# Kernel optimization log

Hardware: AMD Instinct MI355X
Metric: run time of the kernel (lower is better)

Reference implementation:

```python
import jax, jax.numpy as jnp
import numpy as np

B, M = 1024, 200000
D_IN, DIM, D_OUT = 256, 128, 10
T = 1.0
EPS = 1e-7


def setup_inputs() -> dict:
    key = jax.random.key(0)
    k1, k2, k3, k4, k5 = jax.random.split(key, 5)
    x = jax.random.normal(k1, (B, D_IN), dtype=jnp.float32)
    y = jax.random.randint(k2, (B,), 0, D_OUT)
    candidate_x = jax.random.normal(k3, (M, D_IN), dtype=jnp.float32)
    candidate_y = jax.random.randint(k4, (M,), 0, D_OUT)
    W_enc = jax.random.normal(k5, (DIM, D_IN), dtype=jnp.float32) * (1.0 / np.sqrt(D_IN))
    b_enc = jnp.zeros((DIM,), dtype=jnp.float32)
    return {"x": x, "y": y, "candidate_x": candidate_x, "candidate_y": candidate_y,
            "W_enc": W_enc, "b_enc": b_enc, "is_train": 0}


def reference(x, y, candidate_x, candidate_y, W_enc, b_enc, is_train):
    # eval path (is_train == 0): no candidate subsampling, no diagonal masking
    h = x @ W_enc.T + b_enc            # [B, DIM]
    hc = candidate_x @ W_enc.T + b_enc  # [M, DIM]
    # pairwise L2 distance (cdist, p=2)
    sq = jnp.sum(h * h, axis=-1, keepdims=True) + jnp.sum(hc * hc, axis=-1)[None, :] \
         - 2.0 * (h @ hc.T)            # [B, M]
    dist = jnp.sqrt(jnp.maximum(sq, 0.0)) / T
    p = jax.nn.softmax(-dist, axis=-1)  # [B, M]
    y1h = jax.nn.one_hot(candidate_y, D_OUT, dtype=h.dtype)  # [M, D_OUT]
    logits = p @ y1h                    # [B, D_OUT]
    return jnp.log(logits + EPS)
```

## Files before the change

kernel.cpp:

```cpp
#include <hip/hip_runtime.h>
#include <hip/hip_bf16.h>
#include <math.h>

#define B_N   1024
#define M_N   200000
#define DIN   256
#define DIMN  128
#define DOUT  10
#define EPS_F 1e-7f
#define M_PAD 200064
#define NBY   1563
#define NBX_C 1563
#define NBX_X 8
#define CTILES 8
#define NGY   196

typedef __bf16 bf16_t;
typedef __bf16 bf16x8 __attribute__((ext_vector_type(8)));
typedef float  f32x4  __attribute__((ext_vector_type(4)));


__global__ void prep_kernel(const float* __restrict__ W, bf16_t* __restrict__ Wb,
                            const int* __restrict__ cy, int* __restrict__ hist){
    __shared__ int h[DOUT];
    if (threadIdx.x < DOUT) h[threadIdx.x] = 0;
    __syncthreads();
    int gid = blockIdx.x*256 + threadIdx.x;
    if (gid < DIMN*DIN) Wb[gid] = (bf16_t)W[gid];
    for (int i = gid; i < M_N; i += 256*256)
        atomicAdd(&h[cy[i]], 1);
    __syncthreads();
    if (threadIdx.x < DOUT) atomicAdd(&hist[threadIdx.x*16], h[threadIdx.x]);
}

__global__ void prefix_kernel(const int* __restrict__ hist, int* __restrict__ cs){
    if (threadIdx.x == 0 && blockIdx.x == 0){
        int acc = 0;
        for (int c = 0; c < DOUT; ++c){ cs[c] = acc; acc += hist[c*16]; }
        cs[DOUT] = acc;
    }
}


__global__ __launch_bounds__(256) void encode_kernel(
    const float* __restrict__ cx, const float* __restrict__ xx,
    const bf16_t* __restrict__ Wb,
    bf16_t* __restrict__ hcb, bf16_t* __restrict__ hb,
    float* __restrict__ hcn, float* __restrict__ hn,
    const int* __restrict__ cy, int* __restrict__ counters,
    const int* __restrict__ cs)
{
    __shared__ bf16_t As[128][136];
    __shared__ int   posL[128];
    __shared__ float nbuf[128][2];
    __shared__ int   cntL[DOUT], baseL[DOUT];
    const int tid = threadIdx.x;

    const bool isC = (blockIdx.x < NBX_C);
    const float* __restrict__ src = isC ? cx : xx;
    bf16_t* __restrict__ out   = isC ? hcb : hb;
    float*  __restrict__ onorm = isC ? hcn : hn;
    const int N  = isC ? M_N : B_N;
    const int r0 = (isC ? blockIdx.x : blockIdx.x - NBX_C)*128;

    int myc = -1, myrank = 0;
    if (isC){
        if (tid < DOUT) cntL[tid] = 0;
        __syncthreads();
        if (tid < 128 && r0 + tid < N){
            myc = cy[r0 + tid];
            myrank = atomicAdd(&cntL[myc], 1);
        }
        __syncthreads();
        if (tid < DOUT && cntL[tid] > 0)
            baseL[tid] = atomicAdd(&counters[tid*16], cntL[tid]);
        __syncthreads();
    }
    if (tid < 128)
        posL[tid] = (myc >= 0) ? (cs[myc] + baseL[myc] + myrank) : (r0 + tid);

    const int lane = tid & 63, wid = tid >> 6;
    const int wr = wid >> 1, wc = wid & 1;
    const int l15 = lane & 15, quad = lane >> 4;
    const int cbase = wc*64;

    float4 Rlo[8], Rhi[8];
    #pragma unroll
    for (int i = 0; i < 8; ++i){
        int idx = i*256 + tid, row = idx >> 4, col = (idx & 15)*8;
        int rr = r0 + row; if (rr > N-1) rr = N-1;
        const float4* p4 = (const float4*)(src + (size_t)rr*DIN + col);
        Rlo[i] = p4[0]; Rhi[i] = p4[1];
    }
    #pragma unroll
    for (int i = 0; i < 8; ++i){
        int idx = i*256 + tid, row = idx >> 4, col = (idx & 15)*8;
        float4 f0 = Rlo[i], f1 = Rhi[i];
        bf16x8 v;
        v[0]=(bf16_t)f0.x; v[1]=(bf16_t)f0.y; v[2]=(bf16_t)f0.z; v[3]=(bf16_t)f0.w;
        v[4]=(bf16_t)f1.x; v[5]=(bf16_t)f1.y; v[6]=(bf16_t)f1.z; v[7]=(bf16_t)f1.w;
        *(bf16x8*)&As[row][col] = v;
    }
    __syncthreads();
    #pragma unroll
    for (int i = 0; i < 8; ++i){
        int idx = i*256 + tid, row = idx >> 4, col = (idx & 15)*8;
        int rr = r0 + row; if (rr > N-1) rr = N-1;
        const float4* p4 = (const float4*)(src + (size_t)rr*DIN + 128 + col);
        Rlo[i] = p4[0]; Rhi[i] = p4[1];
    }

    f32x4 acc[4][4] = {};
    #pragma unroll
    for (int ks = 0; ks < 4; ++ks){
        const int k = ks*32 + quad*8;
        bf16x8 a[4], b[4];
        #pragma unroll
        for (int rt = 0; rt < 4; ++rt)
            a[rt] = *(const bf16x8*)&As[wr*64 + rt*16 + l15][k];
        #pragma unroll
        for (int ct = 0; ct < 4; ++ct)
            b[ct] = *(const bf16x8*)(Wb + (size_t)(cbase + ct*16 + l15)*DIN + k);
        #pragma unroll
        for (int rt = 0; rt < 4; ++rt)
            #pragma unroll
            for (int ct = 0; ct < 4; ++ct)
                acc[rt][ct] = __builtin_amdgcn_mfma_f32_16x16x32_bf16(a[rt], b[ct], acc[rt][ct], 0, 0, 0);
    }
    __syncthreads();
    #pragma unroll
    for (int i = 0; i < 8; ++i){
        int idx = i*256 + tid, row = idx >> 4, col = (idx & 15)*8;
        float4 f0 = Rlo[i], f1 = Rhi[i];
        bf16x8 v;
        v[0]=(bf16_t)f0.x; v[1]=(bf16_t)f0.y; v[2]=(bf16_t)f0.z; v[3]=(bf16_t)f0.w;
        v[4]=(bf16_t)f1.x; v[5]=(bf16_t)f1.y; v[6]=(bf16_t)f1.z; v[7]=(bf16_t)f1.w;
        *(bf16x8*)&As[row][col] = v;
    }
    __syncthreads();
    #pragma unroll
    for (int ks = 0; ks < 4; ++ks){
        const int k = ks*32 + quad*8;
        bf16x8 a[4], b[4];
        #pragma unroll
        for (int rt = 0; rt < 4; ++rt)
            a[rt] = *(const bf16x8*)&As[wr*64 + rt*16 + l15][k];
        #pragma unroll
        for (int ct = 0; ct < 4; ++ct)
            b[ct] = *(const bf16x8*)(Wb + (size_t)(cbase + ct*16 + l15)*DIN + 128 + k);
        #pragma unroll
        for (int rt = 0; rt < 4; ++rt)
            #pragma unroll
            for (int ct = 0; ct < 4; ++ct)
                acc[rt][ct] = __builtin_amdgcn_mfma_f32_16x16x32_bf16(a[rt], b[ct], acc[rt][ct], 0, 0, 0);
    }

    float np[4][4];
    #pragma unroll
    for (int rt = 0; rt < 4; ++rt)
        #pragma unroll
        for (int r = 0; r < 4; ++r){
            float s = 0.f;
            #pragma unroll
            for (int ct = 0; ct < 4; ++ct){ float v = acc[rt][ct][r]; s += v*v; }
            np[rt][r] = s;
        }
    #pragma unroll
    for (int m = 1; m < 16; m <<= 1)
        #pragma unroll
        for (int rt = 0; rt < 4; ++rt)
            #pragma unroll
            for (int r = 0; r < 4; ++r)
                np[rt][r] += __shfl_xor(np[rt][r], m, 64);
    if (l15 == 0){
        #pragma unroll
        for (int rt = 0; rt < 4; ++rt)
            #pragma unroll
            for (int r = 0; r < 4; ++r)
                nbuf[wr*64 + rt*16 + quad*4 + r][wc] = np[rt][r];
    }

    #pragma unroll
    for (int rt = 0; rt < 4; ++rt){
        #pragma unroll
        for (int r = 0; r < 4; ++r){
            int rl = wr*64 + rt*16 + quad*4 + r;
            if (r0 + rl < N){
                size_t rowp = (size_t)posL[rl]*DIMN;
                #pragma unroll
                for (int ct = 0; ct < 4; ++ct)
                    out[rowp + cbase + ct*16 + l15] = (bf16_t)acc[rt][ct][r];
            }
        }
    }
    __syncthreads();
    if (tid < 128){
        int rs = r0 + tid;
        if (rs < N) onorm[posL[tid]] = nbuf[tid][0] + nbuf[tid][1];
    }
}


__device__ __forceinline__ void bfly16(float (&s)[4][4]){
    #pragma unroll
    for (int m = 1; m < 16; m <<= 1)
        #pragma unroll
        for (int rt = 0; rt < 4; ++rt)
            #pragma unroll
            for (int r = 0; r < 4; ++r)
                s[rt][r] += __shfl_xor(s[rt][r], m, 64);
}

__device__ __forceinline__ void flushC(float (&s)[4][4], int c, int rbase,
                                       int quad, int l15, float* __restrict__ accG){
    bfly16(s);
    if (l15 == 0){
        #pragma unroll
        for (int rt = 0; rt < 4; ++rt)
            #pragma unroll
            for (int r = 0; r < 4; ++r)
                atomicAdd(&accG[(size_t)(rbase + rt*16 + quad*4 + r)*16 + c], s[rt][r]);
    }
}

__global__ __launch_bounds__(256) void fused_kernel(
    const bf16_t* __restrict__ hb, const bf16_t* __restrict__ hcb,
    const float* __restrict__ hn, const float* __restrict__ hcn,
    const int* __restrict__ csg, float* __restrict__ accG)
{
    __shared__ bf16_t Bs[2][128*DIMN];
    const int tid = threadIdx.x;
    const int lane = tid & 63, wid = tid >> 6;
    const int wr = wid >> 1, wc = wid & 1;
    const int l15 = lane & 15, quad = lane >> 4;
    const int rbase = blockIdx.x*128 + wr*64;
    const int lrow = lane >> 4, lpos = lane & 15;

    const int by0 = blockIdx.y*CTILES;
    const int nt  = min(CTILES, NBY - by0);

    bf16x8 a[4][4];
    #pragma unroll
    for (int ks = 0; ks < 4; ++ks)
        #pragma unroll
        for (int rt = 0; rt < 4; ++rt)
            a[ks][rt] = *(const bf16x8*)(hb + (size_t)(rbase + rt*16 + l15)*DIMN + ks*32 + quad*8);

    float hnv[4][4];
    #pragma unroll
    for (int rt = 0; rt < 4; ++rt)
        #pragma unroll
        for (int r = 0; r < 4; ++r)
            hnv[rt][r] = hn[rbase + rt*16 + quad*4 + r];

    int cseg[DOUT+1];
    #pragma unroll
    for (int i = 0; i <= DOUT; ++i) cseg[i] = csg[i];

    auto stage = [&](int buf, int by){
        const size_t gr0 = (size_t)by*128;
        #pragma unroll
        for (int j = 0; j < 8; ++j){
            int g  = wid*8 + j;
            int rl = g*4 + lrow;
            int ck = lpos ^ (rl & 15);
            const bf16_t* gp = hcb + (gr0 + rl)*DIMN + ck*8;
            bf16_t* lp = &Bs[buf][g*512];
            __builtin_amdgcn_global_load_lds(
                (const __attribute__((address_space(1))) void*)gp,
                (__attribute__((address_space(3))) void*)lp, 16, 0, 0);
        }
    };

    stage(0, by0);
    float s[4][4] = {};
    int curC = -1;

    for (int t = 0; t < nt; ++t){
        __syncthreads();
        if (t+1 < nt) stage((t+1)&1, by0 + t + 1);
        const int cbase0 = (by0 + t)*128;
        const bf16_t* bs = Bs[t&1];

        f32x4 acc[4][4] = {};
        #pragma unroll
        for (int ks = 0; ks < 4; ++ks){
            bf16x8 b[4];
            #pragma unroll
            for (int ct = 0; ct < 4; ++ct){
                int cand = wc*64 + ct*16 + l15;
                int p    = (ks*4 + quad) ^ l15;
                b[ct] = *(const bf16x8*)(bs + cand*DIMN + p*8);
            }
            #pragma unroll
            for (int rt = 0; rt < 4; ++rt)
                #pragma unroll
                for (int ct = 0; ct < 4; ++ct)
                    acc[rt][ct] = __builtin_amdgcn_mfma_f32_16x16x32_bf16(a[ks][rt], b[ct], acc[rt][ct], 0, 0, 0);
        }

        float hcnv[4];
        #pragma unroll
        for (int ct = 0; ct < 4; ++ct){
            int cc = cbase0 + wc*64 + ct*16 + l15;
            hcnv[ct] = (cc < M_N) ? hcn[cc] : 1e30f;
        }
        #pragma unroll
        for (int rt = 0; rt < 4; ++rt)
            #pragma unroll
            for (int ct = 0; ct < 4; ++ct)
                #pragma unroll
                for (int r = 0; r < 4; ++r){
                    float sq = fmaxf(hnv[rt][r] + hcnv[ct] - 2.0f*acc[rt][ct][r], 0.0f);
                    acc[rt][ct][r] = __expf(-__builtin_amdgcn_sqrtf(sq));
                }

        const int lastc = min(cbase0 + 127, M_N - 1);
        int cLo = 0, cHi = 0;
        #pragma unroll
        for (int c = 1; c < DOUT; ++c){
            if (cbase0 >= cseg[c]) cLo = c;
            if (lastc  >= cseg[c]) cHi = c;
        }

        if (cLo == curC && cHi == curC){
            #pragma unroll
            for (int rt = 0; rt < 4; ++rt)
                #pragma unroll
                for (int r = 0; r < 4; ++r){
                    float v = 0.f;
                    #pragma unroll
                    for (int ct = 0; ct < 4; ++ct) v += acc[rt][ct][r];
                    s[rt][r] += v;
                }
        } else {
            if (curC >= 0) flushC(s, curC, rbase, quad, l15, accG);
            #pragma unroll
            for (int rt = 0; rt < 4; ++rt)
                #pragma unroll
                for (int r = 0; r < 4; ++r) s[rt][r] = 0.f;
            for (int c = cLo; c <= cHi; ++c){
                const int s0 = cseg[c], s1 = cseg[c+1];
                float m[4][4];
                #pragma unroll
                for (int rt = 0; rt < 4; ++rt)
                    #pragma unroll
                    for (int r = 0; r < 4; ++r){
                        float v = 0.f;
                        #pragma unroll
                        for (int ct = 0; ct < 4; ++ct){
                            int cc = cbase0 + wc*64 + ct*16 + l15;
                            v += (cc >= s0 && cc < s1) ? acc[rt][ct][r] : 0.f;
                        }
                        m[rt][r] = v;
                    }
                if (c == cHi){
                    #pragma unroll
                    for (int rt = 0; rt < 4; ++rt)
                        #pragma unroll
                        for (int r = 0; r < 4; ++r) s[rt][r] = m[rt][r];
                    curC = cHi;
                } else {
                    flushC(m, c, rbase, quad, l15, accG);
                }
            }
        }
    }
    if (curC >= 0) flushC(s, curC, rbase, quad, l15, accG);
}

__global__ void finalize_kernel(const float* __restrict__ accG, float* __restrict__ out){
    int b = blockIdx.x*blockDim.x + threadIdx.x;
    if (b < B_N){
        float v[DOUT]; float den = 0.f;
        #pragma unroll
        for (int c = 0; c < DOUT; ++c){ v[c] = accG[b*16 + c]; den += v[c]; }
        float inv = (den > 0.f) ? 1.0f/den : 0.f;
        #pragma unroll
        for (int c = 0; c < DOUT; ++c) out[b*DOUT + c] = logf(v[c]*inv + EPS_F);
    }
}


extern "C" void kernel_launch(void* const* d_in, const int* in_sizes, int n_in,
                              void* d_out, int out_size, void* d_ws, size_t ws_size,
                              hipStream_t stream)
{
    const float* x  = (const float*)d_in[0];
    const float* cx = (const float*)d_in[2];
    const int*   cy = (const int*)d_in[3];
    const float* W  = (const float*)d_in[4];
    float* out = (float*)d_out;

    char* w = (char*)d_ws;
    size_t off = 0;
    bf16_t* hcb = (bf16_t*)(w + off); off += (size_t)M_PAD*DIMN*2;
    bf16_t* hb  = (bf16_t*)(w + off); off += (size_t)B_N*DIMN*2;
    float*  hcn = (float*) (w + off); off += (size_t)M_PAD*4;
    float*  hn  = (float*) (w + off); off += (size_t)B_N*4;
    bf16_t* Wb  = (bf16_t*)(w + off); off += (size_t)DIMN*DIN*2;
    size_t zoff = off;
    float* accG = (float*)(w + off); off += (size_t)B_N*16*4;
    int* hist     = (int*)(w + off); off += 16*DOUT*4;
    int* counters = (int*)(w + off); off += 16*DOUT*4;
    int* csg      = (int*)(w + off); off += 64;
    size_t zsize = off - zoff;

    hipMemsetAsync(w + zoff, 0, zsize, stream);
    prep_kernel<<<dim3(256), dim3(256), 0, stream>>>(W, Wb, cy, hist);
    prefix_kernel<<<dim3(1), dim3(1), 0, stream>>>(hist, csg);
    encode_kernel<<<dim3(NBX_C + NBX_X), dim3(256), 0, stream>>>(cx, x, Wb, hcb, hb, hcn, hn, cy, counters, csg);
    fused_kernel<<<dim3(B_N/128, NGY), dim3(256), 0, stream>>>(hb, hcb, hn, hcn, csg, accG);
    finalize_kernel<<<dim3((B_N + 255)/256), dim3(256), 0, stream>>>(accG, out);
}
```

Before: 517.9 us.

## Make candidate tiles register-resident and loop over query rows in fused kernel

The fused kernel now gives each block one 128-candidate tile held in registers and loops over all 1024 query rows in 8 groups, reading query encodings straight from global memory (L2-resident) instead of staging candidate tiles through LDS with async loads. This drops the LDS double buffer and the cross-tile class-run accumulation, and sets launch bounds to allow 3 blocks per CU. The prefix kernel is removed, with the class offsets recomputed inline from the histogram in each block, and the accumulator layout is changed to class-major. In exchange, every tile flushes its sums with atomics after each row group, so global atomic traffic goes up.

```diff
diff --git a/kernel.cpp b/kernel.cpp
--- a/kernel.cpp
+++ b/kernel.cpp
@@ -12,8 +12,6 @@
 #define NBY   1563
 #define NBX_C 1563
 #define NBX_X 8
-#define CTILES 8
-#define NGY   196
 
 typedef __bf16 bf16_t;
 typedef __bf16 bf16x8 __attribute__((ext_vector_type(8)));
@@ -31,14 +29,6 @@
         atomicAdd(&h[cy[i]], 1);
     __syncthreads();
     if (threadIdx.x < DOUT) atomicAdd(&hist[threadIdx.x*16], h[threadIdx.x]);
-}
-
-__global__ void prefix_kernel(const int* __restrict__ hist, int* __restrict__ cs){
-    if (threadIdx.x == 0 && blockIdx.x == 0){
-        int acc = 0;
-        for (int c = 0; c < DOUT; ++c){ cs[c] = acc; acc += hist[c*16]; }
-        cs[DOUT] = acc;
-    }
 }
 
 
@@ -48,12 +38,12 @@
     bf16_t* __restrict__ hcb, bf16_t* __restrict__ hb,
     float* __restrict__ hcn, float* __restrict__ hn,
     const int* __restrict__ cy, int* __restrict__ counters,
-    const int* __restrict__ cs)
+    const int* __restrict__ hist)
 {
     __shared__ bf16_t As[128][136];
     __shared__ int   posL[128];
     __shared__ float nbuf[128][2];
-    __shared__ int   cntL[DOUT], baseL[DOUT];
+    __shared__ int   cntL[DOUT], baseL[DOUT], csL[DOUT];
     const int tid = threadIdx.x;
 
     const bool isC = (blockIdx.x < NBX_C);
@@ -66,6 +56,11 @@
     int myc = -1, myrank = 0;
     if (isC){
         if (tid < DOUT) cntL[tid] = 0;
+        if (tid == 0){
+            int a = 0;
+            #pragma unroll
+            for (int c = 0; c < DOUT; ++c){ csL[c] = a; a += hist[c*16]; }
+        }
         __syncthreads();
         if (tid < 128 && r0 + tid < N){
             myc = cy[r0 + tid];
@@ -77,7 +72,7 @@
         __syncthreads();
     }
     if (tid < 128)
-        posL[tid] = (myc >= 0) ? (cs[myc] + baseL[myc] + myrank) : (r0 + tid);
+        posL[tid] = (myc >= 0) ? (csL[myc] + baseL[myc] + myrank) : (r0 + tid);
 
     const int lane = tid & 63, wid = tid >> 6;
     const int wr = wid >> 1, wc = wid & 1;
@@ -211,100 +206,69 @@
                 s[rt][r] += __shfl_xor(s[rt][r], m, 64);
 }
 
-__device__ __forceinline__ void flushC(float (&s)[4][4], int c, int rbase,
-                                       int quad, int l15, float* __restrict__ accG){
-    bfly16(s);
-    if (l15 == 0){
-        #pragma unroll
-        for (int rt = 0; rt < 4; ++rt)
-            #pragma unroll
-            for (int r = 0; r < 4; ++r)
-                atomicAdd(&accG[(size_t)(rbase + rt*16 + quad*4 + r)*16 + c], s[rt][r]);
-    }
-}
-
-__global__ __launch_bounds__(256) void fused_kernel(
+__global__ __launch_bounds__(256, 3) void fused_kernel(
     const bf16_t* __restrict__ hb, const bf16_t* __restrict__ hcb,
     const float* __restrict__ hn, const float* __restrict__ hcn,
-    const int* __restrict__ csg, float* __restrict__ accG)
+    const int* __restrict__ hist, float* __restrict__ accG)
 {
-    __shared__ bf16_t Bs[2][128*DIMN];
     const int tid = threadIdx.x;
     const int lane = tid & 63, wid = tid >> 6;
     const int wr = wid >> 1, wc = wid & 1;
     const int l15 = lane & 15, quad = lane >> 4;
-    const int rbase = blockIdx.x*128 + wr*64;
-    const int lrow = lane >> 4, lpos = lane & 15;
-
-    const int by0 = blockIdx.y*CTILES;
-    const int nt  = min(CTILES, NBY - by0);
-
-    bf16x8 a[4][4];
+    const int cb0 = blockIdx.x*128;
+
+    int cseg[DOUT+1];
+    { int a = 0;
+      #pragma unroll
+      for (int c = 0; c < DOUT; ++c){ cseg[c] = a; a += hist[c*16]; }
+      cseg[DOUT] = a; }
+    const int lastc = min(cb0 + 127, M_N - 1);
+    int cLo = 0, cHi = 0;
+    #pragma unroll
+    for (int c = 1; c < DOUT; ++c){
+        if (cb0  >= cseg[c]) cLo = c;
+        if (lastc >= cseg[c]) cHi = c;
+    }
+
+    bf16x8 b[4][4];
     #pragma unroll
     for (int ks = 0; ks < 4; ++ks)
         #pragma unroll
-        for (int rt = 0; rt < 4; ++rt)
-            a[ks][rt] = *(const bf16x8*)(hb + (size_t)(rbase + rt*16 + l15)*DIMN + ks*32 + quad*8);
-
-    float hnv[4][4];
-    #pragma unroll
-    for (int rt = 0; rt < 4; ++rt)
-        #pragma unroll
-        for (int r = 0; r < 4; ++r)
-            hnv[rt][r] = hn[rbase + rt*16 + quad*4 + r];
-
-    int cseg[DOUT+1];
-    #pragma unroll
-    for (int i = 0; i <= DOUT; ++i) cseg[i] = csg[i];
-
-    auto stage = [&](int buf, int by){
-        const size_t gr0 = (size_t)by*128;
-        #pragma unroll
-        for (int j = 0; j < 8; ++j){
-            int g  = wid*8 + j;
-            int rl = g*4 + lrow;
-            int ck = lpos ^ (rl & 15);
-            const bf16_t* gp = hcb + (gr0 + rl)*DIMN + ck*8;
-            bf16_t* lp = &Bs[buf][g*512];
-            __builtin_amdgcn_global_load_lds(
-                (const __attribute__((address_space(1))) void*)gp,
-                (__attribute__((address_space(3))) void*)lp, 16, 0, 0);
-        }
-    };
-
-    stage(0, by0);
-    float s[4][4] = {};
-    int curC = -1;
-
-    for (int t = 0; t < nt; ++t){
-        __syncthreads();
-        if (t+1 < nt) stage((t+1)&1, by0 + t + 1);
-        const int cbase0 = (by0 + t)*128;
-        const bf16_t* bs = Bs[t&1];
+        for (int ct = 0; ct < 4; ++ct){
+            int cc = cb0 + wc*64 + ct*16 + l15; if (cc > M_N-1) cc = M_N-1;
+            b[ks][ct] = *(const bf16x8*)(hcb + (size_t)cc*DIMN + ks*32 + quad*8);
+        }
+    float hcnv[4];
+    #pragma unroll
+    for (int ct = 0; ct < 4; ++ct){
+        int cc = cb0 + wc*64 + ct*16 + l15;
+        hcnv[ct] = (cc < M_N) ? hcn[cc] : 1e30f;
+    }
+
+    for (int rg = 0; rg < 8; ++rg){
+        const int rbase = rg*128 + wr*64;
 
         f32x4 acc[4][4] = {};
         #pragma unroll
-        for (int ks = 0; ks < 4; ++ks){
-            bf16x8 b[4];
-            #pragma unroll
-            for (int ct = 0; ct < 4; ++ct){
-                int cand = wc*64 + ct*16 + l15;
-                int p    = (ks*4 + quad) ^ l15;
-                b[ct] = *(const bf16x8*)(bs + cand*DIMN + p*8);
-            }
-            #pragma unroll
-            for (int rt = 0; rt < 4; ++rt)
+        for (int rt = 0; rt < 4; ++rt){
+            bf16x8 a[4];
+            #pragma unroll
+            for (int ks = 0; ks < 4; ++ks)
+                a[ks] = *(const bf16x8*)(hb + (size_t)(rbase + rt*16 + l15)*DIMN + ks*32 + quad*8);
+            #pragma unroll
+            for (int ks = 0; ks < 4; ++ks)
                 #pragma unroll
                 for (int ct = 0; ct < 4; ++ct)
-                    acc[rt][ct] = __builtin_amdgcn_mfma_f32_16x16x32_bf16(a[ks][rt], b[ct], acc[rt][ct], 0, 0, 0);
-        }
-
-        float hcnv[4];
-        #pragma unroll
-        for (int ct = 0; ct < 4; ++ct){
-            int cc = cbase0 + wc*64 + ct*16 + l15;
-            hcnv[ct] = (cc < M_N) ? hcn[cc] : 1e30f;
-        }
+                    acc[rt][ct] = __builtin_amdgcn_mfma_f32_16x16x32_bf16(a[ks], b[ks][ct], acc[rt][ct], 0, 0, 0);
+        }
+
+        float hnv[4][4];
+        #pragma unroll
+        for (int rt = 0; rt < 4; ++rt)
+            #pragma unroll
+            for (int r = 0; r < 4; ++r)
+                hnv[rt][r] = hn[rbase + rt*16 + quad*4 + r];
+
         #pragma unroll
         for (int rt = 0; rt < 4; ++rt)
             #pragma unroll
@@ -315,15 +279,8 @@
                     acc[rt][ct][r] = __expf(-__builtin_amdgcn_sqrtf(sq));
                 }
 
-        const int lastc = min(cbase0 + 127, M_N - 1);
-        int cLo = 0, cHi = 0;
-        #pragma unroll
-        for (int c = 1; c < DOUT; ++c){
-            if (cbase0 >= cseg[c]) cLo = c;
-            if (lastc  >= cseg[c]) cHi = c;
-        }
-
-        if (cLo == curC && cHi == curC){
+        if (cLo == cHi){
+            float s[4][4];
             #pragma unroll
             for (int rt = 0; rt < 4; ++rt)
                 #pragma unroll
@@ -331,17 +288,20 @@
                     float v = 0.f;
                     #pragma unroll
                     for (int ct = 0; ct < 4; ++ct) v += acc[rt][ct][r];
-                    s[rt][r] += v;
+                    s[rt][r] = v;
                 }
+            bfly16(s);
+            if (l15 == 0){
+                #pragma unroll
+                for (int rt = 0; rt < 4; ++rt)
+                    #pragma unroll
+                    for (int r = 0; r < 4; ++r)
+                        atomicAdd(&accG[cLo*B_N + rbase + rt*16 + quad*4 + r], s[rt][r]);
+            }
         } else {
-            if (curC >= 0) flushC(s, curC, rbase, quad, l15, accG);
-            #pragma unroll
-            for (int rt = 0; rt < 4; ++rt)
-                #pragma unroll
-                for (int r = 0; r < 4; ++r) s[rt][r] = 0.f;
             for (int c = cLo; c <= cHi; ++c){
                 const int s0 = cseg[c], s1 = cseg[c+1];
-                float m[4][4];
+                float s[4][4];
                 #pragma unroll
                 for (int rt = 0; rt < 4; ++rt)
                     #pragma unroll
@@ -349,24 +309,22 @@
                         float v = 0.f;
                         #pragma unroll
                         for (int ct = 0; ct < 4; ++ct){
-                            int cc = cbase0 + wc*64 + ct*16 + l15;
+                            int cc = cb0 + wc*64 + ct*16 + l15;
                             v += (cc >= s0 && cc < s1) ? acc[rt][ct][r] : 0.f;
                         }
-                        m[rt][r] = v;
+                        s[rt][r] = v;
                     }
-                if (c == cHi){
+                bfly16(s);
+                if (l15 == 0){
                     #pragma unroll
                     for (int rt = 0; rt < 4; ++rt)
                         #pragma unroll
-                        for (int r = 0; r < 4; ++r) s[rt][r] = m[rt][r];
-                    curC = cHi;
-                } else {
-                    flushC(m, c, rbase, quad, l15, accG);
+                        for (int r = 0; r < 4; ++r)
+                            atomicAdd(&accG[c*B_N + rbase + rt*16 + quad*4 + r], s[rt][r]);
                 }
             }
         }
     }
-    if (curC >= 0) flushC(s, curC, rbase, quad, l15, accG);
 }
 
 __global__ void finalize_kernel(const float* __restrict__ accG, float* __restrict__ out){
@@ -374,7 +332,7 @@
     if (b < B_N){
         float v[DOUT]; float den = 0.f;
         #pragma unroll
-        for (int c = 0; c < DOUT; ++c){ v[c] = accG[b*16 + c]; den += v[c]; }
+        for (int c = 0; c < DOUT; ++c){ v[c] = accG[c*B_N + b]; den += v[c]; }
         float inv = (den > 0.f) ? 1.0f/den : 0.f;
         #pragma unroll
         for (int c = 0; c < DOUT; ++c) out[b*DOUT + c] = logf(v[c]*inv + EPS_F);
@@ -400,16 +358,14 @@
     float*  hn  = (float*) (w + off); off += (size_t)B_N*4;
     bf16_t* Wb  = (bf16_t*)(w + off); off += (size_t)DIMN*DIN*2;
     size_t zoff = off;
-    float* accG = (float*)(w + off); off += (size_t)B_N*16*4;
+    float* accG = (float*)(w + off); off += (size_t)DOUT*B_N*4;
     int* hist     = (int*)(w + off); off += 16*DOUT*4;
     int* counters = (int*)(w + off); off += 16*DOUT*4;
-    int* csg      = (int*)(w + off); off += 64;
     size_t zsize = off - zoff;
 
     hipMemsetAsync(w + zoff, 0, zsize, stream);
     prep_kernel<<<dim3(256), dim3(256), 0, stream>>>(W, Wb, cy, hist);
-    prefix_kernel<<<dim3(1), dim3(1), 0, stream>>>(hist, csg);
-    encode_kernel<<<dim3(NBX_C + NBX_X), dim3(256), 0, stream>>>(cx, x, Wb, hcb, hb, hcn, hn, cy, counters, csg);
-    fused_kernel<<<dim3(B_N/128, NGY), dim3(256), 0, stream>>>(hb, hcb, hn, hcn, csg, accG);
+    encode_kernel<<<dim3(NBX_C + NBX_X), dim3(256), 0, stream>>>(cx, x, Wb, hcb, hb, hcn, hn, cy, counters, hist);
+    fused_kernel<<<dim3(NBY), dim3(256), 0, stream>>>(hb, hcb, hn, hcn, hist, accG);
     finalize_kernel<<<dim3((B_N + 255)/256), dim3(256), 0, stream>>>(accG, out);
 }
```

After: 601.0 us. 16.1% more time.
